# Performance work log

Hardware: AMD Instinct MI355X
Metric: run time of the kernel (lower is better)

Reference implementation:

```python
import jax, jax.numpy as jnp
import numpy as np

B, N, CIN, CK, M0 = 2, 4096, 64, 64, 64
NS = 16  # nsample; split into NS//2 cosine + NS//2 euclidean neighbors
LEAKY = 0.1


def _leaky(x):
    return jax.nn.leaky_relu(x, LEAKY)


def _knn_cosine(k, xyz, new_xyz):
    # xyz [B,M,C], new_xyz [B,S,C] -> idx [B,S,k] of smallest cosine distance
    s = new_xyz / jnp.sqrt(jnp.sum(new_xyz ** 2, -1, keepdims=True) + 1e-8)
    d = xyz / jnp.sqrt(jnp.sum(xyz ** 2, -1, keepdims=True) + 1e-8)
    dist = 1.0 - jnp.einsum('bsc,bmc->bsm', s, d)
    return jax.lax.top_k(-dist, k)[1]


def _knn_euclid(k, xyz, new_xyz):
    # squared euclidean distance [B,S,M]
    dist = (jnp.sum(new_xyz ** 2, -1)[:, :, None]
            + jnp.sum(xyz ** 2, -1)[:, None, :]
            - 2.0 * jnp.einsum('bsc,bmc->bsm', new_xyz, xyz))
    return jax.lax.top_k(-dist, k)[1]


def _group(points, idx):
    # points [B,M,C], idx [B,S,K] -> [B,S,K,C]
    return jax.vmap(lambda p, i: p[i])(points, idx)


def _cross(xyz1, xyz2, p1, p2, k1, k2, W_pos, b_pos, W_m1, b_m1, W_m2, b_m2):
    # all point tensors channel-first [B,C,N]; transpose to [B,N,C]
    xyz1t = xyz1.transpose(0, 2, 1)
    xyz2t = xyz2.transpose(0, 2, 1)
    p1t = p1.transpose(0, 2, 1)
    p2t = p2.transpose(0, 2, 1)
    k1t = k1.transpose(0, 2, 1)
    k2t = k2.transpose(0, 2, 1)
    kh = NS // 2
    idx_c = _knn_cosine(kh, k2t, k1t)      # [B,N1,kh] feature-space KNN
    idx_p = _knn_euclid(kh, xyz2t, xyz1t)  # [B,N1,kh] xyz-space KNN
    neighbor_xyz = jnp.concatenate([_group(xyz2t, idx_c), _group(xyz2t, idx_p)], axis=2)  # [B,N1,NS,3]
    direction = neighbor_xyz - xyz1t[:, :, None, :]
    g2 = jnp.concatenate([_group(p2t, idx_c), _group(p2t, idx_p)], axis=2)  # [B,N1,NS,D]
    pos = jnp.einsum('bnkc,dc->bnkd', direction, W_pos) + b_pos  # 1x1 conv on xyz offsets
    new = _leaky(g2 + p1t[:, :, None, :] + pos)  # fused add + leaky relu (bn=Identity)
    new = _leaky(jnp.einsum('bnkd,ed->bnke', new, W_m1) + b_m1)
    new = _leaky(jnp.einsum('bnkd,ed->bnke', new, W_m2) + b_m2)
    new = jnp.max(new, axis=2)  # max-pool over neighbor dim -> [B,N1,D]
    return new.transpose(0, 2, 1)  # [B,D,N1]


def setup_inputs() -> dict:
    key = jax.random.key(0)
    ks = jax.random.split(key, 12)
    rn = lambda k, shape, s=1.0: jax.random.normal(k, shape, jnp.float32) * s
    return {
        'pc1': rn(ks[0], (B, 3, N)),
        'pc2': rn(ks[1], (B, 3, N)),
        'feat1': rn(ks[2], (B, CIN, N)),
        'feat2': rn(ks[3], (B, CIN, N)),
        'knn1': rn(ks[4], (B, CK, N)),
        'knn2': rn(ks[5], (B, CK, N)),
        'W_t11': rn(ks[6], (M0, CIN), 0.1),
        'b_t11': jnp.zeros((M0,), jnp.float32),
        'W_t22': rn(ks[7], (M0, CIN), 0.1),
        'b_t22': jnp.zeros((M0,), jnp.float32),
        'W_pos': rn(ks[8], (M0, 3), 0.1),
        'b_pos': jnp.zeros((M0,), jnp.float32),
        'W_m1': rn(ks[9], (M0, M0), 0.1),
        'b_m1': jnp.zeros((M0,), jnp.float32),
        'W_m2': rn(ks[10], (M0, M0), 0.1),
        'b_m2': jnp.zeros((M0,), jnp.float32),
    }


def reference(pc1, pc2, feat1, feat2, knn1, knn2,
              W_t11, b_t11, W_t22, b_t22, W_pos, b_pos,
              W_m1, b_m1, W_m2, b_m2):
    # cross_t11 / cross_t22: 1x1 Conv1d in_channel -> mlp[0]
    f1a = jnp.einsum('dc,bcn->bdn', W_t11, feat1) + b_t11[None, :, None]
    f2a = jnp.einsum('dc,bcn->bdn', W_t22, feat2) + b_t22[None, :, None]
    f2b = jnp.einsum('dc,bcn->bdn', W_t11, feat2) + b_t11[None, :, None]
    f1b = jnp.einsum('dc,bcn->bdn', W_t22, feat1) + b_t22[None, :, None]
    feat1_new = _cross(pc1, pc2, f1a, f2a, knn1, knn2, W_pos, b_pos, W_m1, b_m1, W_m2, b_m2)
    feat2_new = _cross(pc2, pc1, f2b, f1b, knn2, knn1, W_pos, b_pos, W_m1, b_m1, W_m2, b_m2)
    return (feat1_new, feat2_new)
```

## Files before the change

### kernel.cpp

```cpp
#include <hip/hip_runtime.h>
#include <hip/hip_bf16.h>

#define BB 2
#define NN 4096
#define CH 64

typedef __bf16 bf16x8 __attribute__((ext_vector_type(8)));
typedef float f32x4 __attribute__((ext_vector_type(4)));

__device__ __forceinline__ float lrelu(float v) { return fmaxf(v, 0.1f * v); }
__device__ __forceinline__ float tobf(const __hip_bfloat16& h) { return __bfloat162float(h); }

#define PC1_C 0
#define PC2_C 24576
#define F1_C 49152
#define F2_C 573440
#define K1_C 1097728
#define K2_C 1622016
#define WT11_C 2146304
#define BT11_C 2150400
#define WT22_C 2150464
#define BT22_C 2154560
#define WPOS_C 2154624
#define BPOS_C 2154816
#define WM1_C 2154880
#define BM1_C 2158976
#define WM2_C 2159040
#define BM2_C 2163136
#define CN_TOTAL 2163200

__device__ __forceinline__ unsigned pack_key(float s, int j) {
  __hip_bfloat16 hb = __float2bfloat16(s);
  unsigned h = *reinterpret_cast<unsigned short*>(&hb);
  unsigned m = h ^ (0x8000u | ((h >> 15) * 0x7FFFu));
  return (m << 12) | (unsigned)(4095 - j);
}

__device__ __forceinline__ unsigned umaxu(unsigned a, unsigned b) { return a > b ? a : b; }
__device__ __forceinline__ void casu(unsigned& a, unsigned& b) {
  unsigned mx = a > b ? a : b;
  unsigned mn = a > b ? b : a;
  a = mx; b = mn;
}

__device__ __forceinline__ void merge4(unsigned bd[8], unsigned k0, unsigned k1,
                                       unsigned k2, unsigned k3) {
  casu(k0, k1); casu(k2, k3); casu(k0, k2); casu(k1, k3); casu(k1, k2);
  bd[4] = umaxu(bd[4], k3); bd[5] = umaxu(bd[5], k2);
  bd[6] = umaxu(bd[6], k1); bd[7] = umaxu(bd[7], k0);
  casu(bd[0], bd[4]); casu(bd[1], bd[5]); casu(bd[2], bd[6]); casu(bd[3], bd[7]);
  casu(bd[0], bd[2]); casu(bd[1], bd[3]); casu(bd[4], bd[6]); casu(bd[5], bd[7]);
  casu(bd[0], bd[1]); casu(bd[2], bd[3]); casu(bd[4], bd[5]); casu(bd[6], bd[7]);
}

__global__ void k_detect(const unsigned short* __restrict__ pc1raw, int* __restrict__ flag) {
  int lane = threadIdx.x;
  int bad = 0;
#pragma unroll
  for (int i = 0; i < 64; ++i) {
    unsigned short u = pc1raw[lane * 64 + i];
    int e = (u >> 7) & 0xFF;
    bad += (e >= 140) ? 1 : 0;
  }
#pragma unroll
  for (int s = 32; s; s >>= 1) bad += __shfl_xor(bad, s, 64);
  if (lane == 0) *flag = (bad > 16) ? 1 : 0;
}

__global__ __launch_bounds__(256) void k_ingest(
    const void* p0, const void* p1, const void* p2, const void* p3,
    const void* p4, const void* p5, const void* p6, const void* p7,
    const void* p8, const void* p9, const void* p10, const void* p11,
    const void* p12, const void* p13, const void* p14, const void* p15,
    const int* __restrict__ flag, float* __restrict__ dst) {
  const int cum[17] = {0, 24576, 49152, 573440, 1097728, 1622016, 2146304, 2150400,
                       2150464, 2154560, 2154624, 2154816, 2154880, 2158976, 2159040,
                       2163136, 2163200};
  size_t t = (size_t)blockIdx.x * 256 + threadIdx.x;
  if (t >= (size_t)CN_TOTAL) return;
  int seg = 0;
#pragma unroll
  for (int i = 1; i < 16; ++i) seg += (t >= (size_t)cum[i]) ? 1 : 0;
  size_t local = t - (size_t)cum[seg];
  const void* ptrs[16] = {p0, p1, p2, p3, p4, p5, p6, p7, p8, p9, p10, p11, p12, p13, p14, p15};
  const void* p = ptrs[seg];
  float v;
  if (*flag) v = ((const float*)p)[local];
  else       v = tobf(((const __hip_bfloat16*)p)[local]);
  if (!(v == v) || fabsf(v) > 1e30f) v = 0.f;
  dst[t] = v;
}

__global__ void k_prep_wm(const float* __restrict__ cn, __hip_bfloat16* __restrict__ wmb) {
  int t = blockIdx.x * 256 + threadIdx.x;
  float v = (t < 4096) ? cn[WM1_C + t] : cn[WM2_C + (t - 4096)];
  wmb[t] = __float2bfloat16(v);
}

__global__ __launch_bounds__(256) void k_prep_xyz(const float* __restrict__ cn,
                                                  float4* __restrict__ xyzt) {
  int t = blockIdx.x * 256 + threadIdx.x;
  int n = t & (NN - 1);
  int b = (t >> 12) & 1;
  int a = t >> 13;
  const float* p = cn + (a ? PC2_C : PC1_C) + (size_t)b * 3 * NN + n;
  float x = p[0], y = p[NN], z = p[2 * NN];
  xyzt[(size_t)(a * BB + b) * NN + n] = make_float4(x, y, z, x * x + y * y + z * z);
}

__global__ void k_prep_wpos(const float* __restrict__ cn, float4* __restrict__ wp4) {
  int c = threadIdx.x;
  wp4[c] = make_float4(cn[WPOS_C + 3 * c], cn[WPOS_C + 3 * c + 1], cn[WPOS_C + 3 * c + 2],
                       cn[BPOS_C + c]);
}

__global__ __launch_bounds__(256) void k_prep_knn(const float* __restrict__ cn,
                                                  float* __restrict__ knnt,
                                                  __hip_bfloat16* __restrict__ knnb) {
  int t = blockIdx.x * 256 + threadIdx.x;
  int n = t & (NN - 1);
  int b = (t >> 12) & 1;
  int a = t >> 13;
  const float* col = cn + (a ? K2_C : K1_C) + (size_t)b * CH * NN + n;
  float s = 0.f;
#pragma unroll
  for (int c = 0; c < CH; ++c) { float v = col[(size_t)c * NN]; s += v * v; }
  float inv = 1.0f / sqrtf(s + 1e-8f);
  size_t row = (size_t)(a * BB + b) * NN + n;
  float* o = knnt + row * CH;
  __hip_bfloat16* ob = knnb + row * CH;
#pragma unroll
  for (int c = 0; c < CH; ++c) {
    float v = col[(size_t)c * NN] * inv;
    o[c] = v;
    ob[c] = __float2bfloat16(v);
  }
}

__global__ __launch_bounds__(256) void k_conv(const float* __restrict__ cn,
                                              float* __restrict__ fbuf) {
  __shared__ float wl[CH * CH];
  int bid = blockIdx.x;
  int tile = bid & (NN / 4 - 1);
  int b = (bid >> 10) & 1;
  int sel = bid >> 11;
  const float* W = cn + ((sel == 0 || sel == 2) ? WT11_C : WT22_C);
  const float* bias = cn + ((sel == 0 || sel == 2) ? BT11_C : BT22_C);
  const float* feat = cn + ((sel == 0 || sel == 3) ? F1_C : F2_C);
  int t = threadIdx.x;
#pragma unroll
  for (int i = 0; i < 16; ++i) {
    int e = t * 16 + i;
    wl[(e & 63) * 64 + (e >> 6)] = W[e];
  }
  __syncthreads();
  int p = t >> 6, d = t & 63;
  int n = tile * 4 + p;
  const float* fc = feat + (size_t)b * CH * NN + n;
  float acc = bias[d];
#pragma unroll
  for (int c = 0; c < CH; ++c) acc += wl[c * 64 + d] * fc[(size_t)c * NN];
  fbuf[((size_t)(sel * BB + b) * NN + n) * CH + d] = acc;
}

__global__ __launch_bounds__(512, 4) void k_knn2(const __hip_bfloat16* __restrict__ knnb,
                                                 const float* __restrict__ knnt,
                                                 const float4* __restrict__ xyzt,
                                                 int* __restrict__ idxf) {
  __shared__ unsigned sk[16 * 8 * 33];
  __shared__ int cidx[16 * 16];
  int bid = blockIdx.x;
  int qt = bid & (NN / 16 - 1);
  int b = (bid >> 8) & 1;
  int x = bid >> 9;
  int w = threadIdx.x >> 6;
  int lane = threadIdx.x & 63;
  int lo = lane & 15, g = lane >> 4;
  int q0 = qt * 16;
  int j0 = w * (NN / 8);
  int ss = w * 4 + g;
  int hw = lane >> 5, sl = lane & 31;
  int qq = w * 2 + hw;
  size_t qbase = (size_t)(x * BB + b) * NN;
  size_t dbase = (size_t)((1 - x) * BB + b) * NN;

  unsigned bd[8];

  {
    const __hip_bfloat16* qb = knnb + (qbase + q0) * CH;
    bf16x8 qf0 = *reinterpret_cast<const bf16x8*>(qb + lo * CH + g * 8);
    bf16x8 qf1 = *reinterpret_cast<const bf16x8*>(qb + lo * CH + 32 + g * 8);
    const __hip_bfloat16* db = knnb + dbase * CH;
#pragma unroll
    for (int k = 0; k < 8; ++k) bd[k] = 0u;
#pragma unroll 2
    for (int t = 0; t < 32; ++t) {
      int jb = j0 + t * 16;
      const __hip_bfloat16* ar = db + (size_t)(jb + lo) * CH + g * 8;
      bf16x8 a0 = *reinterpret_cast<const bf16x8*>(ar);
      bf16x8 a1 = *reinterpret_cast<const bf16x8*>(ar + 32);
      f32x4 acc = {0.f, 0.f, 0.f, 0.f};
      acc = __builtin_amdgcn_mfma_f32_16x16x32_bf16(a0, qf0, acc, 0, 0, 0);
      acc = __builtin_amdgcn_mfma_f32_16x16x32_bf16(a1, qf1, acc, 0, 0, 0);
      int mb = jb + g * 4;
      merge4(bd, pack_key(acc[0], mb), pack_key(acc[1], mb + 1),
             pack_key(acc[2], mb + 2), pack_key(acc[3], mb + 3));
    }
  }
#pragma unroll
  for (int k = 0; k < 8; ++k) sk[(lo * 8 + k) * 33 + ss] = bd[k];
  __syncthreads();
  {
    unsigned e[16];
#pragma unroll
    for (int k = 0; k < 8; ++k) e[k] = sk[(qq * 8 + k) * 33 + sl];
#pragma unroll
    for (int k = 8; k < 16; ++k) e[k] = 0u;
#pragma unroll
    for (int s = 1; s < 32; s <<= 1) {
      unsigned f[16];
#pragma unroll
      for (int k = 0; k < 16; ++k) f[k] = (unsigned)__shfl_xor((int)e[k], s, 64);
#pragma unroll
      for (int i = 0; i < 16; ++i) e[i] = umaxu(e[i], f[15 - i]);
      casu(e[0], e[8]); casu(e[1], e[9]); casu(e[2], e[10]); casu(e[3], e[11]);
      casu(e[4], e[12]); casu(e[5], e[13]); casu(e[6], e[14]); casu(e[7], e[15]);
      casu(e[0], e[4]); casu(e[1], e[5]); casu(e[2], e[6]); casu(e[3], e[7]);
      casu(e[8], e[12]); casu(e[9], e[13]); casu(e[10], e[14]); casu(e[11], e[15]);
      casu(e[0], e[2]); casu(e[1], e[3]); casu(e[4], e[6]); casu(e[5], e[7]);
      casu(e[8], e[10]); casu(e[9], e[11]); casu(e[12], e[14]); casu(e[13], e[15]);
      casu(e[0], e[1]); casu(e[2], e[3]); casu(e[4], e[5]); casu(e[6], e[7]);
      casu(e[8], e[9]); casu(e[10], e[11]); casu(e[12], e[13]); casu(e[14], e[15]);
    }
    if (sl == 0) {
#pragma unroll
      for (int k = 0; k < 16; ++k) cidx[qq * 16 + k] = 4095 - (int)(e[k] & 4095u);
    }
    int c = sl >> 1, hr = sl & 1;
    int idx = cidx[qq * 16 + c];
    const float4* qr = reinterpret_cast<const float4*>(knnt + (qbase + q0 + qq) * CH) + hr * 8;
    const float4* dr = reinterpret_cast<const float4*>(knnt + (dbase + idx) * CH) + hr * 8;
    float v = 0.f;
#pragma unroll
    for (int cb = 0; cb < 8; ++cb) {
      float4 qv = qr[cb], dv = dr[cb];
      v += qv.x * dv.x + qv.y * dv.y + qv.z * dv.z + qv.w * dv.w;
    }
    v += __shfl_xor(v, 1, 64);
    float cv = v; int ci = idx; int wsel = 0;
#pragma unroll
    for (int k = 0; k < 8; ++k) {
      float av = cv; int ai = ci;
#pragma unroll
      for (int s = 1; s < 32; s <<= 1) {
        float ov = __shfl_xor(av, s, 64);
        int oi = __shfl_xor(ai, s, 64);
        bool bt = (ov > av) || (ov == av && oi < ai);
        av = bt ? ov : av; ai = bt ? oi : ai;
      }
      if (sl == k) wsel = ai;
      if (ci == ai) cv = -1e38f;
    }
    if (sl < 8) idxf[(qbase + q0 + qq) * 16 + sl] = wsel;
  }

  __syncthreads();
  {
    const float4 q4 = xyzt[qbase + q0 + lo];
    const float4* dbx = xyzt + dbase;
    float tx = 2.f * q4.x, ty = 2.f * q4.y, tz = 2.f * q4.z;
#pragma unroll
    for (int k = 0; k < 8; ++k) bd[k] = 0u;
#pragma unroll 2
    for (int t = 0; t < 32; ++t) {
      int jb = j0 + t * 16 + g * 4;
      float4 p0 = dbx[jb], p1 = dbx[jb + 1], p2 = dbx[jb + 2], p3 = dbx[jb + 3];
      float v0 = fmaf(tx, p0.x, fmaf(ty, p0.y, fmaf(tz, p0.z, -p0.w)));
      float v1 = fmaf(tx, p1.x, fmaf(ty, p1.y, fmaf(tz, p1.z, -p1.w)));
      float v2 = fmaf(tx, p2.x, fmaf(ty, p2.y, fmaf(tz, p2.z, -p2.w)));
      float v3 = fmaf(tx, p3.x, fmaf(ty, p3.y, fmaf(tz, p3.z, -p3.w)));
      merge4(bd, pack_key(v0, jb), pack_key(v1, jb + 1),
             pack_key(v2, jb + 2), pack_key(v3, jb + 3));
    }
  }
#pragma unroll
  for (int k = 0; k < 8; ++k) sk[(lo * 8 + k) * 33 + ss] = bd[k];
  __syncthreads();
  {
    unsigned e[16];
#pragma unroll
    for (int k = 0; k < 8; ++k) e[k] = sk[(qq * 8 + k) * 33 + sl];
#pragma unroll
    for (int k = 8; k < 16; ++k) e[k] = 0u;
#pragma unroll
    for (int s = 1; s < 32; s <<= 1) {
      unsigned f[16];
#pragma unroll
      for (int k = 0; k < 16; ++k) f[k] = (unsigned)__shfl_xor((int)e[k], s, 64);
#pragma unroll
      for (int i = 0; i < 16; ++i) e[i] = umaxu(e[i], f[15 - i]);
      casu(e[0], e[8]); casu(e[1], e[9]); casu(e[2], e[10]); casu(e[3], e[11]);
      casu(e[4], e[12]); casu(e[5], e[13]); casu(e[6], e[14]); casu(e[7], e[15]);
      casu(e[0], e[4]); casu(e[1], e[5]); casu(e[2], e[6]); casu(e[3], e[7]);
      casu(e[8], e[12]); casu(e[9], e[13]); casu(e[10], e[14]); casu(e[11], e[15]);
      casu(e[0], e[2]); casu(e[1], e[3]); casu(e[4], e[6]); casu(e[5], e[7]);
      casu(e[8], e[10]); casu(e[9], e[11]); casu(e[12], e[14]); casu(e[13], e[15]);
      casu(e[0], e[1]); casu(e[2], e[3]); casu(e[4], e[5]); casu(e[6], e[7]);
      casu(e[8], e[9]); casu(e[10], e[11]); casu(e[12], e[13]); casu(e[14], e[15]);
    }
    if (sl == 0) {
#pragma unroll
      for (int k = 0; k < 16; ++k) cidx[qq * 16 + k] = 4095 - (int)(e[k] & 4095u);
    }
    int c = sl >> 1;
    int idx = cidx[qq * 16 + c];
    const float4 q4 = xyzt[qbase + q0 + qq];
    float4 p = xyzt[dbase + idx];
    float v = fmaf(2.f * q4.x, p.x, fmaf(2.f * q4.y, p.y, fmaf(2.f * q4.z, p.z, -p.w)));
    float cv = v; int ci = idx; int wsel = 0;
#pragma unroll
    for (int k = 0; k < 8; ++k) {
      float av = cv; int ai = ci;
#pragma unroll
      for (int s = 1; s < 32; s <<= 1) {
        float ov = __shfl_xor(av, s, 64);
        int oi = __shfl_xor(ai, s, 64);
        bool bt = (ov > av) || (ov == av && oi < ai);
        av = bt ? ov : av; ai = bt ? oi : ai;
      }
      if (sl == k) wsel = ai;
      if (ci == ai) cv = -1e38f;
    }
    if (sl < 8) idxf[(qbase + q0 + qq) * 16 + 8 + sl] = wsel;
  }
}

__global__ __launch_bounds__(256) void k_mlp(const float* __restrict__ fbuf,
                                             const float4* __restrict__ xyzt,
                                             const int* __restrict__ idxf,
                                             const float4* __restrict__ wp4,
                                             const __hip_bfloat16* __restrict__ wmb,
                                             const float* __restrict__ cn,
                                             float* __restrict__ out) {
  __shared__ __bf16 h1s[4 * 16 * 72];
  const int t = threadIdx.x;
  const int wv = t >> 6, L = t & 63;
  const int lo = L & 15, g = L >> 4;
  int bid = blockIdx.x;
  const int qt = bid & (NN / 4 - 1);
  const int b = (bid >> 10) & 1;
  const int x = bid >> 11;
  const int q = qt * 4 + wv;

  bf16x8 w1f[4][2], w2f[4][2];
#pragma unroll
  for (int tt = 0; tt < 4; ++tt)
#pragma unroll
    for (int kc = 0; kc < 2; ++kc) {
      int e = tt * 16 + lo, c0 = kc * 32 + g * 8;
      w1f[tt][kc] = *reinterpret_cast<const bf16x8*>(wmb + e * 64 + c0);
      w2f[tt][kc] = *reinterpret_cast<const bf16x8*>(wmb + 4096 + e * 64 + c0);
    }

  const float* pq  = fbuf + ((size_t)((x ? 2 : 0) * BB + b)) * NN * CH;
  const float* pdb = fbuf + ((size_t)((x ? 3 : 1) * BB + b)) * NN * CH;
  const float4* qx  = xyzt + (size_t)(x * BB + b) * NN;
  const float4* dbx = xyzt + (size_t)((1 - x) * BB + b) * NN;

  const int m = lo;
  int jm = idxf[(((size_t)x * BB + b) * NN + q) * 16 + m];
  jm &= (NN - 1);
  const float4 q4 = qx[q];
  const float4 p4 = dbx[jm];
  const float dx = p4.x - q4.x, dy = p4.y - q4.y, dz = p4.z - q4.z;
  const float* g2p = pdb + (size_t)jm * CH;
  const float* pqp = pq + (size_t)q * CH;

  bf16x8 a0, a1;
#pragma unroll
  for (int kc = 0; kc < 2; ++kc) {
#pragma unroll
    for (int j = 0; j < 8; ++j) {
      int c = kc * 32 + g * 8 + j;
      float4 wp = wp4[c];
      float v = g2p[c] + pqp[c] + wp.x * dx + wp.y * dy + wp.z * dz + wp.w;
      v = lrelu(v);
      if (kc == 0) a0[j] = (__bf16)v; else a1[j] = (__bf16)v;
    }
  }

  __bf16* hrow = h1s + wv * 16 * 72;
#pragma unroll
  for (int tt = 0; tt < 4; ++tt) {
    float bv = cn[BM1_C + tt * 16 + lo];
    f32x4 acc = {bv, bv, bv, bv};
    acc = __builtin_amdgcn_mfma_f32_16x16x32_bf16(a0, w1f[tt][0], acc, 0, 0, 0);
    acc = __builtin_amdgcn_mfma_f32_16x16x32_bf16(a1, w1f[tt][1], acc, 0, 0, 0);
#pragma unroll
    for (int r = 0; r < 4; ++r) {
      float v = lrelu(acc[r]);
      hrow[(g * 4 + r) * 72 + tt * 16 + lo] = (__bf16)v;
    }
  }
  __syncthreads();
  bf16x8 h1a = *reinterpret_cast<const bf16x8*>(hrow + m * 72 + g * 8);
  bf16x8 h1b = *reinterpret_cast<const bf16x8*>(hrow + m * 72 + 32 + g * 8);

  size_t obase = ((size_t)(x * BB + b) * CH) * NN;
#pragma unroll
  for (int tt = 0; tt < 4; ++tt) {
    float bv = cn[BM2_C + tt * 16 + lo];
    f32x4 acc = {bv, bv, bv, bv};
    acc = __builtin_amdgcn_mfma_f32_16x16x32_bf16(h1a, w2f[tt][0], acc, 0, 0, 0);
    acc = __builtin_amdgcn_mfma_f32_16x16x32_bf16(h1b, w2f[tt][1], acc, 0, 0, 0);
    float v = fmaxf(fmaxf(lrelu(acc[0]), lrelu(acc[1])), fmaxf(lrelu(acc[2]), lrelu(acc[3])));
    v = fmaxf(v, __shfl_xor(v, 16, 64));
    v = fmaxf(v, __shfl_xor(v, 32, 64));
    if (g == 0) out[obase + (size_t)(tt * 16 + lo) * NN + q] = v;
  }
}

#define CN_OFF 0
#define FB_OFF ((size_t)CN_TOTAL)
#define KT_OFF (FB_OFF + (size_t)4 * BB * NN * CH)
#define XZ_OFF (KT_OFF + (size_t)2 * BB * NN * CH)
#define WP4_OFF (XZ_OFF + (size_t)2 * BB * NN * 4)
#define WMB_OFF (WP4_OFF + 256)
#define IDX_OFF (WMB_OFF + 4096)
#define FLAG_OFF (IDX_OFF + 262144)
#define KNB_OFF (FLAG_OFF + 4)

extern "C" void kernel_launch(void* const* d_in, const int* in_sizes, int n_in,
                              void* d_out, int out_size, void* d_ws, size_t ws_size,
                              hipStream_t stream) {
  float* ws = (float*)d_ws;
  float* cn = ws + CN_OFF;
  int* flag = (int*)(ws + FLAG_OFF);

  k_detect<<<1, 64, 0, stream>>>((const unsigned short*)d_in[0], flag);
  k_ingest<<<(CN_TOTAL + 255) / 256, 256, 0, stream>>>(
      d_in[0], d_in[1], d_in[2], d_in[3], d_in[4], d_in[5], d_in[6], d_in[7],
      d_in[8], d_in[9], d_in[10], d_in[11], d_in[12], d_in[13], d_in[14], d_in[15],
      flag, cn);
  k_prep_wm<<<32, 256, 0, stream>>>(cn, (__hip_bfloat16*)(ws + WMB_OFF));
  k_prep_xyz<<<(2 * BB * NN) / 256, 256, 0, stream>>>(cn, (float4*)(ws + XZ_OFF));
  k_prep_wpos<<<1, 64, 0, stream>>>(cn, (float4*)(ws + WP4_OFF));
  k_prep_knn<<<(2 * BB * NN) / 256, 256, 0, stream>>>(cn, ws + KT_OFF,
                                                     (__hip_bfloat16*)(ws + KNB_OFF));
  k_conv<<<4 * BB * (NN / 4), 256, 0, stream>>>(cn, ws + FB_OFF);
  k_knn2<<<2 * BB * (NN / 16), 512, 0, stream>>>(
      (const __hip_bfloat16*)(ws + KNB_OFF), ws + KT_OFF,
      (const float4*)(ws + XZ_OFF), (int*)(ws + IDX_OFF));
  k_mlp<<<2 * BB * (NN / 4), 256, 0, stream>>>(ws + FB_OFF, (const float4*)(ws + XZ_OFF),
                                               (const int*)(ws + IDX_OFF), (const float4*)(ws + WP4_OFF),
                                               (const __hip_bfloat16*)(ws + WMB_OFF), cn,
                                               (float*)d_out);
}
```

Measured before the change: 314.4 us.

## Fuse cosine and euclidean KNN scans, merge prep kernels, vectorize MLP gathers

The cosine and euclidean candidate scans now run in one pass over each database tile, so the tile loop and its xyz loads are shared and a block barrier is dropped. Each scan keeps two independent top-8 lists per thread, which are merged at the end to shorten the dependency chains. Sort keys are now built from float bits plus a 12-bit index instead of a bf16 round-trip, which keeps more score precision. Three small prep kernels become one launch, and the MLP kernel loads its gathered feature rows with float4 instead of scalar reads. The cost is higher register pressure from four live top-8 arrays plus a second shared buffer, which may lower occupancy.

```diff
diff --git a/kernel.cpp b/kernel.cpp
--- a/kernel.cpp
+++ b/kernel.cpp
@@ -29,11 +29,9 @@
 #define BM2_C 2163136
 #define CN_TOTAL 2163200
 
-__device__ __forceinline__ unsigned pack_key(float s, int j) {
-  __hip_bfloat16 hb = __float2bfloat16(s);
-  unsigned h = *reinterpret_cast<unsigned short*>(&hb);
-  unsigned m = h ^ (0x8000u | ((h >> 15) * 0x7FFFu));
-  return (m << 12) | (unsigned)(4095 - j);
+__device__ __forceinline__ unsigned fmap(float s) {
+  unsigned u = __float_as_uint(s);
+  return u ^ ((unsigned)((int)u >> 31) | 0x80000000u);
 }
 
 __device__ __forceinline__ unsigned umaxu(unsigned a, unsigned b) { return a > b ? a : b; }
@@ -43,14 +41,26 @@
   a = mx; b = mn;
 }
 
+__device__ __forceinline__ void bitonic8(unsigned bd[8]) {
+  casu(bd[0], bd[4]); casu(bd[1], bd[5]); casu(bd[2], bd[6]); casu(bd[3], bd[7]);
+  casu(bd[0], bd[2]); casu(bd[1], bd[3]); casu(bd[4], bd[6]); casu(bd[5], bd[7]);
+  casu(bd[0], bd[1]); casu(bd[2], bd[3]); casu(bd[4], bd[5]); casu(bd[6], bd[7]);
+}
+
 __device__ __forceinline__ void merge4(unsigned bd[8], unsigned k0, unsigned k1,
                                        unsigned k2, unsigned k3) {
   casu(k0, k1); casu(k2, k3); casu(k0, k2); casu(k1, k3); casu(k1, k2);
   bd[4] = umaxu(bd[4], k3); bd[5] = umaxu(bd[5], k2);
   bd[6] = umaxu(bd[6], k1); bd[7] = umaxu(bd[7], k0);
-  casu(bd[0], bd[4]); casu(bd[1], bd[5]); casu(bd[2], bd[6]); casu(bd[3], bd[7]);
-  casu(bd[0], bd[2]); casu(bd[1], bd[3]); casu(bd[4], bd[6]); casu(bd[5], bd[7]);
-  casu(bd[0], bd[1]); casu(bd[2], bd[3]); casu(bd[4], bd[5]); casu(bd[6], bd[7]);
+  bitonic8(bd);
+}
+
+__device__ __forceinline__ void merge88(unsigned a[8], const unsigned b[8]) {
+  a[0] = umaxu(a[0], b[7]); a[1] = umaxu(a[1], b[6]);
+  a[2] = umaxu(a[2], b[5]); a[3] = umaxu(a[3], b[4]);
+  a[4] = umaxu(a[4], b[3]); a[5] = umaxu(a[5], b[2]);
+  a[6] = umaxu(a[6], b[1]); a[7] = umaxu(a[7], b[0]);
+  bitonic8(a);
 }
 
 __global__ void k_detect(const unsigned short* __restrict__ pc1raw, int* __restrict__ flag) {
@@ -91,27 +101,29 @@
   dst[t] = v;
 }
 
-__global__ void k_prep_wm(const float* __restrict__ cn, __hip_bfloat16* __restrict__ wmb) {
-  int t = blockIdx.x * 256 + threadIdx.x;
-  float v = (t < 4096) ? cn[WM1_C + t] : cn[WM2_C + (t - 4096)];
-  wmb[t] = __float2bfloat16(v);
-}
-
-__global__ __launch_bounds__(256) void k_prep_xyz(const float* __restrict__ cn,
-                                                  float4* __restrict__ xyzt) {
-  int t = blockIdx.x * 256 + threadIdx.x;
-  int n = t & (NN - 1);
-  int b = (t >> 12) & 1;
-  int a = t >> 13;
-  const float* p = cn + (a ? PC2_C : PC1_C) + (size_t)b * 3 * NN + n;
-  float x = p[0], y = p[NN], z = p[2 * NN];
-  xyzt[(size_t)(a * BB + b) * NN + n] = make_float4(x, y, z, x * x + y * y + z * z);
-}
-
-__global__ void k_prep_wpos(const float* __restrict__ cn, float4* __restrict__ wp4) {
-  int c = threadIdx.x;
-  wp4[c] = make_float4(cn[WPOS_C + 3 * c], cn[WPOS_C + 3 * c + 1], cn[WPOS_C + 3 * c + 2],
-                       cn[BPOS_C + c]);
+__global__ __launch_bounds__(256) void k_prep_misc(const float* __restrict__ cn,
+                                                   __hip_bfloat16* __restrict__ wmb,
+                                                   float4* __restrict__ xyzt,
+                                                   float4* __restrict__ wp4) {
+  int bid = blockIdx.x;
+  if (bid < 32) {
+    int t = bid * 256 + threadIdx.x;
+    float v = (t < 4096) ? cn[WM1_C + t] : cn[WM2_C + (t - 4096)];
+    wmb[t] = __float2bfloat16(v);
+  } else if (bid < 96) {
+    int t = (bid - 32) * 256 + threadIdx.x;
+    int n = t & (NN - 1);
+    int b = (t >> 12) & 1;
+    int a = t >> 13;
+    const float* p = cn + (a ? PC2_C : PC1_C) + (size_t)b * 3 * NN + n;
+    float x = p[0], y = p[NN], z = p[2 * NN];
+    xyzt[(size_t)(a * BB + b) * NN + n] = make_float4(x, y, z, x * x + y * y + z * z);
+  } else {
+    int c = threadIdx.x;
+    if (c < 64)
+      wp4[c] = make_float4(cn[WPOS_C + 3 * c], cn[WPOS_C + 3 * c + 1],
+                           cn[WPOS_C + 3 * c + 2], cn[BPOS_C + c]);
+  }
 }
 
 __global__ __launch_bounds__(256) void k_prep_knn(const float* __restrict__ cn,
@@ -163,11 +175,12 @@
   fbuf[((size_t)(sel * BB + b) * NN + n) * CH + d] = acc;
 }
 
-__global__ __launch_bounds__(512, 4) void k_knn2(const __hip_bfloat16* __restrict__ knnb,
+__global__ __launch_bounds__(512, 4) void k_knn3(const __hip_bfloat16* __restrict__ knnb,
                                                  const float* __restrict__ knnt,
                                                  const float4* __restrict__ xyzt,
                                                  int* __restrict__ idxf) {
-  __shared__ unsigned sk[16 * 8 * 33];
+  __shared__ unsigned skc[16 * 8 * 33];
+  __shared__ unsigned ske[16 * 8 * 33];
   __shared__ int cidx[16 * 16];
   int bid = blockIdx.x;
   int qt = bid & (NN / 16 - 1);
@@ -184,36 +197,59 @@
   size_t qbase = (size_t)(x * BB + b) * NN;
   size_t dbase = (size_t)((1 - x) * BB + b) * NN;
 
-  unsigned bd[8];
-
-  {
-    const __hip_bfloat16* qb = knnb + (qbase + q0) * CH;
-    bf16x8 qf0 = *reinterpret_cast<const bf16x8*>(qb + lo * CH + g * 8);
-    bf16x8 qf1 = *reinterpret_cast<const bf16x8*>(qb + lo * CH + 32 + g * 8);
-    const __hip_bfloat16* db = knnb + dbase * CH;
-#pragma unroll
-    for (int k = 0; k < 8; ++k) bd[k] = 0u;
-#pragma unroll 2
-    for (int t = 0; t < 32; ++t) {
-      int jb = j0 + t * 16;
-      const __hip_bfloat16* ar = db + (size_t)(jb + lo) * CH + g * 8;
-      bf16x8 a0 = *reinterpret_cast<const bf16x8*>(ar);
-      bf16x8 a1 = *reinterpret_cast<const bf16x8*>(ar + 32);
-      f32x4 acc = {0.f, 0.f, 0.f, 0.f};
-      acc = __builtin_amdgcn_mfma_f32_16x16x32_bf16(a0, qf0, acc, 0, 0, 0);
-      acc = __builtin_amdgcn_mfma_f32_16x16x32_bf16(a1, qf1, acc, 0, 0, 0);
-      int mb = jb + g * 4;
-      merge4(bd, pack_key(acc[0], mb), pack_key(acc[1], mb + 1),
-             pack_key(acc[2], mb + 2), pack_key(acc[3], mb + 3));
-    }
-  }
-#pragma unroll
-  for (int k = 0; k < 8; ++k) sk[(lo * 8 + k) * 33 + ss] = bd[k];
+  const __hip_bfloat16* qb = knnb + (qbase + q0) * CH;
+  bf16x8 qf0 = *reinterpret_cast<const bf16x8*>(qb + lo * CH + g * 8);
+  bf16x8 qf1 = *reinterpret_cast<const bf16x8*>(qb + lo * CH + 32 + g * 8);
+  const __hip_bfloat16* db = knnb + dbase * CH;
+  const float4 q4 = xyzt[qbase + q0 + lo];
+  const float4* dbx = xyzt + dbase;
+  float tx = 2.f * q4.x, ty = 2.f * q4.y, tz = 2.f * q4.z;
+
+  unsigned bc0[8], bc1[8], be0[8], be1[8];
+#pragma unroll
+  for (int k = 0; k < 8; ++k) { bc0[k] = 0u; bc1[k] = 0u; be0[k] = 0u; be1[k] = 0u; }
+
+  auto TILE = [&](unsigned (&bc)[8], unsigned (&be)[8], int jb) {
+    unsigned rc = (unsigned)(4095 - jb - g * 4);
+    const __hip_bfloat16* ar = db + (size_t)(jb + lo) * CH + g * 8;
+    bf16x8 a0 = *reinterpret_cast<const bf16x8*>(ar);
+    bf16x8 a1 = *reinterpret_cast<const bf16x8*>(ar + 32);
+    f32x4 acc = {0.f, 0.f, 0.f, 0.f};
+    acc = __builtin_amdgcn_mfma_f32_16x16x32_bf16(a0, qf0, acc, 0, 0, 0);
+    acc = __builtin_amdgcn_mfma_f32_16x16x32_bf16(a1, qf1, acc, 0, 0, 0);
+    int je = jb + g * 4;
+    float4 p0 = dbx[je], p1 = dbx[je + 1], p2 = dbx[je + 2], p3 = dbx[je + 3];
+    float v0 = fmaf(tx, p0.x, fmaf(ty, p0.y, fmaf(tz, p0.z, -p0.w)));
+    float v1 = fmaf(tx, p1.x, fmaf(ty, p1.y, fmaf(tz, p1.z, -p1.w)));
+    float v2 = fmaf(tx, p2.x, fmaf(ty, p2.y, fmaf(tz, p2.z, -p2.w)));
+    float v3 = fmaf(tx, p3.x, fmaf(ty, p3.y, fmaf(tz, p3.z, -p3.w)));
+    merge4(bc, (__float_as_uint(acc[0] + 4.0f) & 0xFFFFF000u) | rc,
+               (__float_as_uint(acc[1] + 4.0f) & 0xFFFFF000u) | (rc - 1),
+               (__float_as_uint(acc[2] + 4.0f) & 0xFFFFF000u) | (rc - 2),
+               (__float_as_uint(acc[3] + 4.0f) & 0xFFFFF000u) | (rc - 3));
+    merge4(be, (fmap(v0) & 0xFFFFF000u) | rc,
+               (fmap(v1) & 0xFFFFF000u) | (rc - 1),
+               (fmap(v2) & 0xFFFFF000u) | (rc - 2),
+               (fmap(v3) & 0xFFFFF000u) | (rc - 3));
+  };
+
+  for (int t = 0; t < 16; ++t) {
+    TILE(bc0, be0, j0 + (2 * t) * 16);
+    TILE(bc1, be1, j0 + (2 * t + 1) * 16);
+  }
+  merge88(bc0, bc1);
+  merge88(be0, be1);
+#pragma unroll
+  for (int k = 0; k < 8; ++k) {
+    skc[(lo * 8 + k) * 33 + ss] = bc0[k];
+    ske[(lo * 8 + k) * 33 + ss] = be0[k];
+  }
   __syncthreads();
+
   {
     unsigned e[16];
 #pragma unroll
-    for (int k = 0; k < 8; ++k) e[k] = sk[(qq * 8 + k) * 33 + sl];
+    for (int k = 0; k < 8; ++k) e[k] = skc[(qq * 8 + k) * 33 + sl];
 #pragma unroll
     for (int k = 8; k < 16; ++k) e[k] = 0u;
 #pragma unroll
@@ -241,7 +277,7 @@
     const float4* qr = reinterpret_cast<const float4*>(knnt + (qbase + q0 + qq) * CH) + hr * 8;
     const float4* dr = reinterpret_cast<const float4*>(knnt + (dbase + idx) * CH) + hr * 8;
     float v = 0.f;
-#pragma unroll
+#pragma unroll 4
     for (int cb = 0; cb < 8; ++cb) {
       float4 qv = qr[cb], dv = dr[cb];
       v += qv.x * dv.x + qv.y * dv.y + qv.z * dv.z + qv.w * dv.w;
@@ -264,32 +300,10 @@
     if (sl < 8) idxf[(qbase + q0 + qq) * 16 + sl] = wsel;
   }
 
-  __syncthreads();
-  {
-    const float4 q4 = xyzt[qbase + q0 + lo];
-    const float4* dbx = xyzt + dbase;
-    float tx = 2.f * q4.x, ty = 2.f * q4.y, tz = 2.f * q4.z;
-#pragma unroll
-    for (int k = 0; k < 8; ++k) bd[k] = 0u;
-#pragma unroll 2
-    for (int t = 0; t < 32; ++t) {
-      int jb = j0 + t * 16 + g * 4;
-      float4 p0 = dbx[jb], p1 = dbx[jb + 1], p2 = dbx[jb + 2], p3 = dbx[jb + 3];
-      float v0 = fmaf(tx, p0.x, fmaf(ty, p0.y, fmaf(tz, p0.z, -p0.w)));
-      float v1 = fmaf(tx, p1.x, fmaf(ty, p1.y, fmaf(tz, p1.z, -p1.w)));
-      float v2 = fmaf(tx, p2.x, fmaf(ty, p2.y, fmaf(tz, p2.z, -p2.w)));
-      float v3 = fmaf(tx, p3.x, fmaf(ty, p3.y, fmaf(tz, p3.z, -p3.w)));
-      merge4(bd, pack_key(v0, jb), pack_key(v1, jb + 1),
-             pack_key(v2, jb + 2), pack_key(v3, jb + 3));
-    }
-  }
-#pragma unroll
-  for (int k = 0; k < 8; ++k) sk[(lo * 8 + k) * 33 + ss] = bd[k];
-  __syncthreads();
   {
     unsigned e[16];
 #pragma unroll
-    for (int k = 0; k < 8; ++k) e[k] = sk[(qq * 8 + k) * 33 + sl];
+    for (int k = 0; k < 8; ++k) e[k] = ske[(qq * 8 + k) * 33 + sl];
 #pragma unroll
     for (int k = 8; k < 16; ++k) e[k] = 0u;
 #pragma unroll
@@ -314,9 +328,9 @@
     }
     int c = sl >> 1;
     int idx = cidx[qq * 16 + c];
-    const float4 q4 = xyzt[qbase + q0 + qq];
+    const float4 qx4 = xyzt[qbase + q0 + qq];
     float4 p = xyzt[dbase + idx];
-    float v = fmaf(2.f * q4.x, p.x, fmaf(2.f * q4.y, p.y, fmaf(2.f * q4.z, p.z, -p.w)));
+    float v = fmaf(2.f * qx4.x, p.x, fmaf(2.f * qx4.y, p.y, fmaf(2.f * qx4.z, p.z, -p.w)));
     float cv = v; int ci = idx; int wsel = 0;
 #pragma unroll
     for (int k = 0; k < 8; ++k) {
@@ -373,8 +387,18 @@
   const float4 q4 = qx[q];
   const float4 p4 = dbx[jm];
   const float dx = p4.x - q4.x, dy = p4.y - q4.y, dz = p4.z - q4.z;
-  const float* g2p = pdb + (size_t)jm * CH;
-  const float* pqp = pq + (size_t)q * CH;
+
+  const float4* g2v = reinterpret_cast<const float4*>(pdb + (size_t)jm * CH);
+  const float4* pqv = reinterpret_cast<const float4*>(pq + (size_t)q * CH);
+  float hv[16];
+  {
+    float4 t0 = g2v[g * 2], t1 = g2v[g * 2 + 1], t2 = g2v[g * 2 + 8], t3 = g2v[g * 2 + 9];
+    float4 u0 = pqv[g * 2], u1 = pqv[g * 2 + 1], u2 = pqv[g * 2 + 8], u3 = pqv[g * 2 + 9];
+    hv[0] = t0.x + u0.x; hv[1] = t0.y + u0.y; hv[2] = t0.z + u0.z; hv[3] = t0.w + u0.w;
+    hv[4] = t1.x + u1.x; hv[5] = t1.y + u1.y; hv[6] = t1.z + u1.z; hv[7] = t1.w + u1.w;
+    hv[8] = t2.x + u2.x; hv[9] = t2.y + u2.y; hv[10] = t2.z + u2.z; hv[11] = t2.w + u2.w;
+    hv[12] = t3.x + u3.x; hv[13] = t3.y + u3.y; hv[14] = t3.z + u3.z; hv[15] = t3.w + u3.w;
+  }
 
   bf16x8 a0, a1;
 #pragma unroll
@@ -383,7 +407,7 @@
     for (int j = 0; j < 8; ++j) {
       int c = kc * 32 + g * 8 + j;
       float4 wp = wp4[c];
-      float v = g2p[c] + pqp[c] + wp.x * dx + wp.y * dy + wp.z * dz + wp.w;
+      float v = hv[kc * 8 + j] + wp.x * dx + wp.y * dy + wp.z * dz + wp.w;
       v = lrelu(v);
       if (kc == 0) a0[j] = (__bf16)v; else a1[j] = (__bf16)v;
     }
@@ -442,13 +466,12 @@
       d_in[0], d_in[1], d_in[2], d_in[3], d_in[4], d_in[5], d_in[6], d_in[7],
       d_in[8], d_in[9], d_in[10], d_in[11], d_in[12], d_in[13], d_in[14], d_in[15],
       flag, cn);
-  k_prep_wm<<<32, 256, 0, stream>>>(cn, (__hip_bfloat16*)(ws + WMB_OFF));
-  k_prep_xyz<<<(2 * BB * NN) / 256, 256, 0, stream>>>(cn, (float4*)(ws + XZ_OFF));
-  k_prep_wpos<<<1, 64, 0, stream>>>(cn, (float4*)(ws + WP4_OFF));
+  k_prep_misc<<<97, 256, 0, stream>>>(cn, (__hip_bfloat16*)(ws + WMB_OFF),
+                                      (float4*)(ws + XZ_OFF), (float4*)(ws + WP4_OFF));
   k_prep_knn<<<(2 * BB * NN) / 256, 256, 0, stream>>>(cn, ws + KT_OFF,
                                                      (__hip_bfloat16*)(ws + KNB_OFF));
   k_conv<<<4 * BB * (NN / 4), 256, 0, stream>>>(cn, ws + FB_OFF);
-  k_knn2<<<2 * BB * (NN / 16), 512, 0, stream>>>(
+  k_knn3<<<2 * BB * (NN / 16), 512, 0, stream>>>(
       (const __hip_bfloat16*)(ws + KNB_OFF), ws + KT_OFF,
       (const float4*)(ws + XZ_OFF), (int*)(ws + IDX_OFF));
   k_mlp<<<2 * BB * (NN / 4), 256, 0, stream>>>(ws + FB_OFF, (const float4*)(ws + XZ_OFF),
```

After: 311.7 us. No clear change (-0.9%).
